# Optimization experiments

Measured on AMD Instinct MI355X. Metric: run time of the kernel, lower is better.

The kernel has to match this reference:

```python
import jax, jax.numpy as jnp
import numpy as np

DIM = 2048
H = 256
N_HEADS = 4
HEAD_DIM = H // N_HEADS
N_SIG = 6
SW_HID = 2 * DIM  # SwiGLU(dim, dim*2)
B, S = 4, 2048
EPS = 1e-6


def _rmsnorm(v, w):
    return v * jax.lax.rsqrt(jnp.mean(v * v, axis=-1, keepdims=True) + EPS) * w


def setup_inputs() -> dict:
    key = jax.random.key(0)
    ks = jax.random.split(key, 32)
    sc = 0.02
    inp = {
        'x': jax.random.normal(ks[0], (B, S, DIM), jnp.float32),
        'epistemic': jax.random.uniform(ks[1], (B, 64), jnp.float32),
        'aleatoric': jax.random.uniform(ks[2], (B, 64), jnp.float32),
        'ood_score': jax.random.uniform(ks[3], (B,), jnp.float32),
        'conformal_unc': jax.random.uniform(ks[4], (B,), jnp.float32),
        'ece': jax.random.uniform(ks[5], (1,), jnp.float32),
        'moral_std': jax.random.uniform(ks[6], (B,), jnp.float32),
        # signal_proj: Linear(1, h)
        'sp_w': jax.random.normal(ks[7], (H, 1), jnp.float32) * sc,
        'sp_b': jnp.zeros((H,), jnp.float32),
        # MultiheadAttention packed qkv + out proj
        'in_proj_w': jax.random.normal(ks[8], (3 * H, H), jnp.float32) * sc,
        'in_proj_b': jnp.zeros((3 * H,), jnp.float32),
        'out_w': jax.random.normal(ks[9], (H, H), jnp.float32) * sc,
        'out_b': jnp.zeros((H,), jnp.float32),
        # confidence_head: Linear(6,h) -> GELU -> Linear(h,1) -> Sigmoid
        'ch_w1': jax.random.normal(ks[10], (H, N_SIG), jnp.float32) * sc,
        'ch_b1': jnp.zeros((H,), jnp.float32),
        'ch_w2': jax.random.normal(ks[11], (1, H), jnp.float32) * sc,
        'ch_b2': jnp.zeros((1,), jnp.float32),
        # summary_proj: Linear(h,dim) -> RMSNorm -> SwiGLU(dim, 2*dim) -> Linear(dim,dim) -> RMSNorm
        'sum_w1': jax.random.normal(ks[12], (DIM, H), jnp.float32) * sc,
        'sum_b1': jnp.zeros((DIM,), jnp.float32),
        'rms1_w': jnp.ones((DIM,), jnp.float32),
        'sw_w1': jax.random.normal(ks[13], (SW_HID, DIM), jnp.float32) * sc,
        'sw_w3': jax.random.normal(ks[14], (SW_HID, DIM), jnp.float32) * sc,
        'sw_w2': jax.random.normal(ks[15], (DIM, SW_HID), jnp.float32) * sc,
        'sum_w2': jax.random.normal(ks[16], (DIM, DIM), jnp.float32) * sc,
        'sum_b2': jnp.zeros((DIM,), jnp.float32),
        'rms2_w': jnp.ones((DIM,), jnp.float32),
        # final norm
        'norm_w': jnp.ones((DIM,), jnp.float32),
    }
    return inp


def reference(x, epistemic, aleatoric, ood_score, conformal_unc, ece, moral_std,
              sp_w, sp_b, in_proj_w, in_proj_b, out_w, out_b,
              ch_w1, ch_b1, ch_w2, ch_b2,
              sum_w1, sum_b1, rms1_w, sw_w1, sw_w3, sw_w2, sum_w2, sum_b2, rms2_w,
              norm_w):
    b, s, d = x.shape
    # [B, 6] stack of scalar uncertainty signals
    signals = jnp.stack([
        epistemic.mean(-1), aleatoric.mean(-1), ood_score, conformal_unc,
        jnp.broadcast_to(ece, (b,)), moral_std], axis=-1)
    # confidence head: Linear -> GELU(exact) -> Linear -> Sigmoid
    c = jax.nn.gelu(signals @ ch_w1.T + ch_b1, approximate=False)
    confidence = jax.nn.sigmoid(c @ ch_w2.T + ch_b2)[..., 0]
    # project each scalar signal to h dims: [B, 6, H]
    sp = signals[..., None] * sp_w[:, 0] + sp_b
    # self-attention over the 6 signal tokens
    qkv = sp @ in_proj_w.T + in_proj_b            # [B, 6, 3H]
    q, k, v = jnp.split(qkv, 3, axis=-1)
    q = q.reshape(b, N_SIG, N_HEADS, HEAD_DIM)
    k = k.reshape(b, N_SIG, N_HEADS, HEAD_DIM)
    v = v.reshape(b, N_SIG, N_HEADS, HEAD_DIM)
    scores = jnp.einsum('bqhd,bkhd->bhqk', q, k) / jnp.sqrt(jnp.float32(HEAD_DIM))
    attn = jax.nn.softmax(scores, axis=-1)
    o = jnp.einsum('bhqk,bkhd->bqhd', attn, v).reshape(b, N_SIG, H)
    o = o @ out_w.T + out_b
    unc_summary = o.mean(axis=1)                   # [B, H]
    # summary_proj applied (as in the original) to the [B*S, H] expanded rows
    u = jnp.broadcast_to(unc_summary[:, None, :], (b, s, H)).reshape(b * s, H)
    t = u @ sum_w1.T + sum_b1                      # [B*S, DIM]
    t = _rmsnorm(t, rms1_w)
    t = (jax.nn.silu(t @ sw_w1.T) * (t @ sw_w3.T)) @ sw_w2.T  # SwiGLU
    t = t @ sum_w2.T + sum_b2
    unc_embedding = _rmsnorm(t, rms2_w).reshape(b, s, d)
    x_aware = _rmsnorm(x + unc_embedding * 0.05, norm_w)
    return (x_aware, confidence, signals, unc_embedding)
```

## Files before the change

kernel.cpp:

```cpp
#include <hip/hip_runtime.h>
#include <math.h>

#define DIMN 2048
#define HDIM 256
#define NSIG 6
#define NHEADS 4
#define HEADDIM 64
#define SWHID 4096
#define BB 4
#define SSEQ 2048
#define EPSF 1e-6f

__device__ __forceinline__ float wsum(float v) {
    #pragma unroll
    for (int m = 1; m < 64; m <<= 1) v += __shfl_xor(v, m, 64);
    return v;
}

__device__ __forceinline__ float dot4(float4 a, float4 b) {
    return a.x*b.x + a.y*b.y + a.z*b.z + a.w*b.w;
}

__global__ __launch_bounds__(256) void k0_ac(
    const float* __restrict__ ipw, const float* __restrict__ ipb,
    const float* __restrict__ spw, const float* __restrict__ spb,
    float* __restrict__ A, float* __restrict__ C, float* __restrict__ accum)
{
    int t = threadIdx.x, wv = t >> 6, lane = t & 63;
    if (blockIdx.x == 0 && t < 8) accum[t] = 0.f;
    int r = blockIdx.x * 4 + wv;
    float4 w  = ((const float4*)(ipw + (size_t)r * HDIM))[lane];
    float4 a4 = ((const float4*)spw)[lane];
    float4 b4 = ((const float4*)spb)[lane];
    float aa = wsum(dot4(w, a4));
    float cc = wsum(dot4(w, b4));
    if (lane == 0) { A[r] = aa; C[r] = cc + ipb[r]; }
}

__global__ __launch_bounds__(256) void kUV(
    const float* __restrict__ A, const float* __restrict__ C,
    const float* __restrict__ outw,
    float* __restrict__ U, float* __restrict__ V)
{
    int t = threadIdx.x, wv = t >> 6, lane = t & 63;
    int n = blockIdx.x * 4 + wv;
    float4 w = ((const float4*)(outw + (size_t)n * HDIM))[lane];
    float4 a = ((const float4*)(A + 512))[lane];
    float4 c = ((const float4*)(C + 512))[lane];
    float pu = dot4(w, a), pv = dot4(w, c);
    #pragma unroll
    for (int m = 1; m < 16; m <<= 1) {
        pu += __shfl_xor(pu, m, 64);
        pv += __shfl_xor(pv, m, 64);
    }
    if ((lane & 15) == 0) {
        int h = lane >> 4;
        U[n * NHEADS + h] = pu;
        V[n * NHEADS + h] = pv;
    }
}

__global__ __launch_bounds__(256) void kB_front(
    const float* __restrict__ epi, const float* __restrict__ ale,
    const float* __restrict__ ood, const float* __restrict__ cunc,
    const float* __restrict__ ece, const float* __restrict__ moral,
    const float* __restrict__ chw1, const float* __restrict__ chb1,
    const float* __restrict__ chw2, const float* __restrict__ chb2,
    const float* __restrict__ A, const float* __restrict__ C,
    const float* __restrict__ U, const float* __restrict__ V,
    const float* __restrict__ outb,
    float* __restrict__ us, float* __restrict__ out_conf,
    float* __restrict__ out_sig)
{
    __shared__ float sA[512], sC[512];
    __shared__ float sSig[BB][NSIG];
    __shared__ float sGram[NHEADS][4];
    __shared__ float sAtt[BB][NHEADS][NSIG][NSIG];
    __shared__ float sBar[BB][NHEADS][NSIG];
    __shared__ float sRedW[BB][4];
    int t = threadIdx.x, wv = t >> 6, lane = t & 63;

    for (int r = t; r < 512; r += 256) { sA[r] = A[r]; sC[r] = C[r]; }

    {
        int b = wv;
        float se = wsum(epi[b * 64 + lane]) * (1.f / 64.f);
        float sa = wsum(ale[b * 64 + lane]) * (1.f / 64.f);
        if (lane == 0) {
            sSig[b][0] = se; sSig[b][1] = sa;
            sSig[b][2] = ood[b]; sSig[b][3] = cunc[b];
            sSig[b][4] = ece[0]; sSig[b][5] = moral[b];
            #pragma unroll
            for (int k = 0; k < NSIG; k++) out_sig[b * NSIG + k] = sSig[b][k];
        }
    }
    __syncthreads();

    {
        int h = wv;
        float aq = sA[h * 64 + lane],       cq = sC[h * 64 + lane];
        float ak = sA[256 + h * 64 + lane], ck = sC[256 + h * 64 + lane];
        float g0 = wsum(aq * ak);
        float g1 = wsum(aq * ck);
        float g2 = wsum(cq * ak);
        float g3 = wsum(cq * ck);
        if (lane == 0) { sGram[h][0] = g0; sGram[h][1] = g1; sGram[h][2] = g2; sGram[h][3] = g3; }
    }

    {
        float c1[NSIG];
        #pragma unroll
        for (int j = 0; j < NSIG; j++) c1[j] = chw1[t * NSIG + j];
        float cb = chb1[t], cw2 = chw2[t];
        #pragma unroll
        for (int b = 0; b < BB; b++) {
            float z = cb;
            #pragma unroll
            for (int j = 0; j < NSIG; j++) z += sSig[b][j] * c1[j];
            float g = 0.5f * z * (1.f + erff(z * 0.70710678118654752f));
            float v = wsum(g * cw2);
            if (lane == 0) sRedW[b][wv] = v;
        }
    }
    __syncthreads();
    if (t < BB) {
        float s = sRedW[t][0] + sRedW[t][1] + sRedW[t][2] + sRedW[t][3] + chb2[0];
        out_conf[t] = 1.f / (1.f + expf(-s));
    }

    if (t < 96) {
        int b = t / 24, r = t % 24, h = r / 6, qi = r % 6;
        float sq = sSig[b][qi];
        float g0 = sGram[h][0], g1 = sGram[h][1], g2 = sGram[h][2], g3 = sGram[h][3];
        float sc[NSIG]; float mx = -1e30f;
        #pragma unroll
        for (int ki = 0; ki < NSIG; ki++) {
            float sk = sSig[b][ki];
            float s = (g0 * sq * sk + g1 * sq + g2 * sk + g3) * 0.125f;
            sc[ki] = s; mx = fmaxf(mx, s);
        }
        float den = 0;
        #pragma unroll
        for (int ki = 0; ki < NSIG; ki++) { sc[ki] = expf(sc[ki] - mx); den += sc[ki]; }
        float inv = 1.f / den;
        #pragma unroll
        for (int ki = 0; ki < NSIG; ki++) sAtt[b][h][qi][ki] = sc[ki] * inv;
    }
    __syncthreads();

    if (t < 96) {
        int b = t / 24, r = t % 24, h = r / 6, ki = r % 6;
        float s = 0;
        #pragma unroll
        for (int qi = 0; qi < NSIG; qi++) s += sAtt[b][h][qi][ki];
        sBar[b][h][ki] = s * (1.f / 6.f);
    }
    __syncthreads();

    {
        float uu[NHEADS], vv[NHEADS];
        #pragma unroll
        for (int h = 0; h < NHEADS; h++) {
            uu[h] = U[t * NHEADS + h];
            vv[h] = V[t * NHEADS + h];
        }
        float ob = outb[t];
        #pragma unroll
        for (int b = 0; b < BB; b++) {
            float acc = ob;
            #pragma unroll
            for (int h = 0; h < NHEADS; h++) {
                float hu = 0, hv = 0;
                #pragma unroll
                for (int ki = 0; ki < NSIG; ki++) {
                    hu += sBar[b][h][ki] * sSig[b][ki];
                    hv += sBar[b][h][ki];
                }
                acc += hu * uu[h] + hv * vv[h];
            }
            us[b * HDIM + t] = acc;
        }
    }
}

__global__ __launch_bounds__(256) void k2_sumproj(
    const float* __restrict__ us, const float* __restrict__ w1,
    const float* __restrict__ b1, const float* __restrict__ rw1,
    float* __restrict__ t1n, float* __restrict__ accum)
{
    __shared__ float bsq[BB];
    int t = threadIdx.x, wv = t >> 6, lane = t & 63;
    if (t < BB) bsq[t] = 0.f;
    __syncthreads();
    int d = blockIdx.x * 4 + wv;
    float4 w = ((const float4*)(w1 + (size_t)d * HDIM))[lane];
    float acc[BB];
    #pragma unroll
    for (int b = 0; b < BB; b++) {
        float4 u = ((const float4*)(us + b * HDIM))[lane];
        acc[b] = dot4(w, u);
    }
    #pragma unroll
    for (int b = 0; b < BB; b++) acc[b] = wsum(acc[b]);
    if (lane == 0) {
        #pragma unroll
        for (int b = 0; b < BB; b++) {
            float v = acc[b] + b1[d];
            atomicAdd(&bsq[b], v * v);
            t1n[b * DIMN + d] = v * rw1[d];
        }
    }
    __syncthreads();
    if (t < BB) atomicAdd(&accum[t], bsq[t]);
}

__global__ __launch_bounds__(256) void k3_swiglu(
    const float* __restrict__ t1n, const float* __restrict__ sw1,
    const float* __restrict__ sw3, const float* __restrict__ accum,
    float* __restrict__ h)
{
    __shared__ __align__(16) float sT[BB * DIMN];
    int t = threadIdx.x, wv = t >> 6, lane = t & 63;
    #pragma unroll
    for (int k = 0; k < 8; k++)
        ((float4*)sT)[k * 256 + t] = ((const float4*)t1n)[k * 256 + t];
    __syncthreads();
    int j = blockIdx.x * 4 + wv;
    const float4* r1 = (const float4*)(sw1 + (size_t)j * DIMN);
    const float4* r3 = (const float4*)(sw3 + (size_t)j * DIMN);
    float acc1[BB] = {0,0,0,0}, acc3[BB] = {0,0,0,0};
    #pragma unroll
    for (int it = 0; it < 8; it++) {
        float4 w1 = r1[it * 64 + lane];
        float4 w3 = r3[it * 64 + lane];
        #pragma unroll
        for (int b = 0; b < BB; b++) {
            float4 tv = ((const float4*)(sT + b * DIMN))[it * 64 + lane];
            acc1[b] += dot4(w1, tv);
            acc3[b] += dot4(w3, tv);
        }
    }
    #pragma unroll
    for (int b = 0; b < BB; b++) { acc1[b] = wsum(acc1[b]); acc3[b] = wsum(acc3[b]); }
    if (lane == 0) {
        #pragma unroll
        for (int b = 0; b < BB; b++) {
            float s = rsqrtf(accum[b] * (1.f / DIMN) + EPSF);
            float a = acc1[b] * s;
            float sil = a / (1.f + expf(-a));
            h[b * SWHID + j] = sil * (acc3[b] * s);
        }
    }
}

__global__ __launch_bounds__(256) void k4_down(
    const float* __restrict__ h, const float* __restrict__ sw2,
    float* __restrict__ t2)
{
    __shared__ __align__(16) float sH[BB * SWHID];
    int t = threadIdx.x, wv = t >> 6, lane = t & 63;
    #pragma unroll
    for (int k = 0; k < 16; k++)
        ((float4*)sH)[k * 256 + t] = ((const float4*)h)[k * 256 + t];
    __syncthreads();
    int d = blockIdx.x * 4 + wv;
    const float4* wr = (const float4*)(sw2 + (size_t)d * SWHID);
    float acc[BB] = {0,0,0,0};
    #pragma unroll
    for (int it = 0; it < 16; it++) {
        float4 w = wr[it * 64 + lane];
        #pragma unroll
        for (int b = 0; b < BB; b++) {
            float4 hv = ((const float4*)(sH + b * SWHID))[it * 64 + lane];
            acc[b] += dot4(w, hv);
        }
    }
    #pragma unroll
    for (int b = 0; b < BB; b++) acc[b] = wsum(acc[b]);
    if (lane == 0) {
        #pragma unroll
        for (int b = 0; b < BB; b++) t2[b * DIMN + d] = acc[b];
    }
}

__global__ __launch_bounds__(256) void k5_out(
    const float* __restrict__ t2, const float* __restrict__ w2,
    const float* __restrict__ b2, const float* __restrict__ rw2,
    float* __restrict__ t3n, float* __restrict__ accum)
{
    __shared__ __align__(16) float sT[BB * DIMN];
    __shared__ float bsq[BB];
    int t = threadIdx.x, wv = t >> 6, lane = t & 63;
    if (t < BB) bsq[t] = 0.f;
    #pragma unroll
    for (int k = 0; k < 8; k++)
        ((float4*)sT)[k * 256 + t] = ((const float4*)t2)[k * 256 + t];
    __syncthreads();
    int d = blockIdx.x * 4 + wv;
    const float4* wr = (const float4*)(w2 + (size_t)d * DIMN);
    float acc[BB] = {0,0,0,0};
    #pragma unroll
    for (int it = 0; it < 8; it++) {
        float4 w = wr[it * 64 + lane];
        #pragma unroll
        for (int b = 0; b < BB; b++) {
            float4 tv = ((const float4*)(sT + b * DIMN))[it * 64 + lane];
            acc[b] += dot4(w, tv);
        }
    }
    #pragma unroll
    for (int b = 0; b < BB; b++) acc[b] = wsum(acc[b]);
    if (lane == 0) {
        #pragma unroll
        for (int b = 0; b < BB; b++) {
            float v = acc[b] + b2[d];
            atomicAdd(&bsq[b], v * v);
            t3n[b * DIMN + d] = v * rw2[d];
        }
    }
    __syncthreads();
    if (t < BB) atomicAdd(&accum[4 + t], bsq[t]);
}

__global__ __launch_bounds__(256) void k7_final(
    const float* __restrict__ x, const float* __restrict__ t3n,
    const float* __restrict__ accum, const float* __restrict__ nw,
    float* __restrict__ xa, float* __restrict__ ue)
{
    int t = threadIdx.x, wv = t >> 6, lane = t & 63;
    size_t row = (size_t)blockIdx.x * 4 + wv;
    int b = (int)(row >> 11);
    float scale2 = rsqrtf(accum[4 + b] * (1.f / DIMN) + EPSF);
    const float4* xr = (const float4*)(x + row * DIMN);
    const float4* tr = (const float4*)(t3n + (size_t)b * DIMN);
    float4 e[8], y[8];
    float ss = 0.f;
    #pragma unroll
    for (int k = 0; k < 8; k++) {
        int idx = k * 64 + lane;
        float4 tv = tr[idx];
        float4 xv = xr[idx];
        e[k].x = tv.x * scale2; e[k].y = tv.y * scale2;
        e[k].z = tv.z * scale2; e[k].w = tv.w * scale2;
        y[k].x = xv.x + 0.05f * e[k].x; y[k].y = xv.y + 0.05f * e[k].y;
        y[k].z = xv.z + 0.05f * e[k].z; y[k].w = xv.w + 0.05f * e[k].w;
        ss += dot4(y[k], y[k]);
    }
    float rs = rsqrtf(wsum(ss) * (1.f / DIMN) + EPSF);
    float4* xo = (float4*)(xa + row * DIMN);
    float4* uo = (float4*)(ue + row * DIMN);
    #pragma unroll
    for (int k = 0; k < 8; k++) {
        int idx = k * 64 + lane;
        float4 nv = ((const float4*)nw)[idx];
        float4 o;
        o.x = y[k].x * rs * nv.x; o.y = y[k].y * rs * nv.y;
        o.z = y[k].z * rs * nv.z; o.w = y[k].w * rs * nv.w;
        xo[idx] = o;
        uo[idx] = e[k];
    }
}

extern "C" void kernel_launch(void* const* d_in, const int* in_sizes, int n_in,
                              void* d_out, int out_size, void* d_ws, size_t ws_size,
                              hipStream_t stream)
{
    (void)in_sizes; (void)n_in; (void)out_size; (void)ws_size;
    const float* x     = (const float*)d_in[0];
    const float* epi   = (const float*)d_in[1];
    const float* ale   = (const float*)d_in[2];
    const float* ood   = (const float*)d_in[3];
    const float* cunc  = (const float*)d_in[4];
    const float* ece   = (const float*)d_in[5];
    const float* moral = (const float*)d_in[6];
    const float* spw   = (const float*)d_in[7];
    const float* spb   = (const float*)d_in[8];
    const float* ipw   = (const float*)d_in[9];
    const float* ipb   = (const float*)d_in[10];
    const float* outw  = (const float*)d_in[11];
    const float* outb  = (const float*)d_in[12];
    const float* chw1  = (const float*)d_in[13];
    const float* chb1  = (const float*)d_in[14];
    const float* chw2  = (const float*)d_in[15];
    const float* chb2  = (const float*)d_in[16];
    const float* sumw1 = (const float*)d_in[17];
    const float* sumb1 = (const float*)d_in[18];
    const float* rms1  = (const float*)d_in[19];
    const float* sww1  = (const float*)d_in[20];
    const float* sww3  = (const float*)d_in[21];
    const float* sww2  = (const float*)d_in[22];
    const float* sumw2 = (const float*)d_in[23];
    const float* sumb2 = (const float*)d_in[24];
    const float* rms2  = (const float*)d_in[25];
    const float* normw = (const float*)d_in[26];

    float* out  = (float*)d_out;
    float* xa   = out;
    float* conf = out + (size_t)BB * SSEQ * DIMN;
    float* sig  = conf + BB;
    float* ue   = sig + BB * NSIG;

    float* ws    = (float*)d_ws;
    float* A     = ws;
    float* C     = ws + 768;
    float* U     = ws + 1536;
    float* V     = ws + 2560;
    float* us    = ws + 3584;
    float* t1n   = ws + 4608;
    float* h     = ws + 12800;
    float* t2    = ws + 29184;
    float* t3n   = ws + 37376;
    float* accum = ws + 45568;

    k0_ac   <<<192, 256, 0, stream>>>(ipw, ipb, spw, spb, A, C, accum);
    kUV     <<<64, 256, 0, stream>>>(A, C, outw, U, V);
    kB_front<<<1, 256, 0, stream>>>(epi, ale, ood, cunc, ece, moral,
                                    chw1, chb1, chw2, chb2, A, C, U, V, outb,
                                    us, conf, sig);
    k2_sumproj<<<512, 256, 0, stream>>>(us, sumw1, sumb1, rms1, t1n, accum);
    k3_swiglu <<<1024, 256, 0, stream>>>(t1n, sww1, sww3, accum, h);
    k4_down   <<<512, 256, 0, stream>>>(h, sww2, t2);
    k5_out    <<<512, 256, 0, stream>>>(t2, sumw2, sumb2, rms2, t3n, accum);
    k7_final  <<<2048, 256, 0, stream>>>(x, t3n, accum, normw, xa, ue);
}
```

Before: 354.1 us.

## Fuse weight-chain kernels into one persistent kernel with grid barriers and prefetch

Merges the front attention, sum projection, SwiGLU, down projection and output projection kernels into a single 512-block persistent kernel. Stages are separated by atomic grid-wide barriers, and idle warps in the early small stages prefetch the SwiGLU weights into cache. The out-projection is reorganised to go through a head-weighted vector g followed by one matvec. This removes several kernel launch gaps and overlaps weight loading with the serial front work. In exchange it depends on all 512 blocks being co-resident (launch bounds of 2 blocks per CU), which risks deadlock, and adds the cost of the spin barriers.

```diff
diff --git a/kernel.cpp b/kernel.cpp
--- a/kernel.cpp
+++ b/kernel.cpp
@@ -10,6 +10,7 @@
 #define BB 4
 #define SSEQ 2048
 #define EPSF 1e-6f
+#define NBLK 512
 
 __device__ __forceinline__ float wsum(float v) {
     #pragma unroll
@@ -21,305 +22,319 @@
     return a.x*b.x + a.y*b.y + a.z*b.z + a.w*b.w;
 }
 
-__global__ __launch_bounds__(256) void k0_ac(
-    const float* __restrict__ ipw, const float* __restrict__ ipb,
-    const float* __restrict__ spw, const float* __restrict__ spb,
-    float* __restrict__ A, float* __restrict__ C, float* __restrict__ accum)
+__device__ __forceinline__ void gsync(unsigned* bar) {
+    __syncthreads();
+    if (threadIdx.x == 0) {
+        __hip_atomic_fetch_add(bar, 1u, __ATOMIC_RELEASE,
+                               __HIP_MEMORY_SCOPE_AGENT);
+        while (__hip_atomic_load(bar, __ATOMIC_ACQUIRE,
+                                 __HIP_MEMORY_SCOPE_AGENT) < NBLK) {
+            __builtin_amdgcn_s_sleep(2);
+        }
+    }
+    __syncthreads();
+}
+
+struct Params {
+    const float *ipw, *ipb, *spw, *spb;
+    const float *epi, *ale, *ood, *cunc, *ece, *moral;
+    const float *chw1, *chb1, *chw2, *chb2;
+    const float *outw, *outb;
+    const float *sumw1, *sumb1, *rms1;
+    const float *sww1, *sww3, *sww2;
+    const float *sumw2, *sumb2, *rms2;
+    float *A, *C, *g, *us, *t1n, *h, *t2, *t3n, *accum;
+    float *conf, *sig;
+    unsigned *bar;
+};
+
+__global__ __launch_bounds__(256) void kinit(float* accum, unsigned* bar) {
+    int t = threadIdx.x;
+    if (t < 8) accum[t] = 0.f;
+    bar[t] = 0u;
+}
+
+__device__ __forceinline__ void pf8k(const float* sww1, const float* sww3,
+                                     int c, int lane) {
+    if (c >= 8192) return;
+    const float* base = (c < 4096) ? (sww1 + (size_t)c * 2048)
+                                   : (sww3 + (size_t)(c - 4096) * 2048);
+    const float4* p4 = (const float4*)base;
+    float s = 0.f;
+    #pragma unroll
+    for (int k = 0; k < 8; k++) {
+        float4 v = p4[k * 64 + lane];
+        s += v.x + v.y + v.z + v.w;
+    }
+    asm volatile("" :: "v"(s));
+}
+
+__global__ __launch_bounds__(256, 2) void kchain(Params p)
 {
+    __shared__ __align__(16) float smem[16384];
     int t = threadIdx.x, wv = t >> 6, lane = t & 63;
-    if (blockIdx.x == 0 && t < 8) accum[t] = 0.f;
-    int r = blockIdx.x * 4 + wv;
-    float4 w  = ((const float4*)(ipw + (size_t)r * HDIM))[lane];
-    float4 a4 = ((const float4*)spw)[lane];
-    float4 b4 = ((const float4*)spb)[lane];
-    float aa = wsum(dot4(w, a4));
-    float cc = wsum(dot4(w, b4));
-    if (lane == 0) { A[r] = aa; C[r] = cc + ipb[r]; }
-}
-
-__global__ __launch_bounds__(256) void kUV(
-    const float* __restrict__ A, const float* __restrict__ C,
-    const float* __restrict__ outw,
-    float* __restrict__ U, float* __restrict__ V)
-{
-    int t = threadIdx.x, wv = t >> 6, lane = t & 63;
-    int n = blockIdx.x * 4 + wv;
-    float4 w = ((const float4*)(outw + (size_t)n * HDIM))[lane];
-    float4 a = ((const float4*)(A + 512))[lane];
-    float4 c = ((const float4*)(C + 512))[lane];
-    float pu = dot4(w, a), pv = dot4(w, c);
-    #pragma unroll
-    for (int m = 1; m < 16; m <<= 1) {
-        pu += __shfl_xor(pu, m, 64);
-        pv += __shfl_xor(pv, m, 64);
-    }
-    if ((lane & 15) == 0) {
-        int h = lane >> 4;
-        U[n * NHEADS + h] = pu;
-        V[n * NHEADS + h] = pv;
-    }
-}
-
-__global__ __launch_bounds__(256) void kB_front(
-    const float* __restrict__ epi, const float* __restrict__ ale,
-    const float* __restrict__ ood, const float* __restrict__ cunc,
-    const float* __restrict__ ece, const float* __restrict__ moral,
-    const float* __restrict__ chw1, const float* __restrict__ chb1,
-    const float* __restrict__ chw2, const float* __restrict__ chb2,
-    const float* __restrict__ A, const float* __restrict__ C,
-    const float* __restrict__ U, const float* __restrict__ V,
-    const float* __restrict__ outb,
-    float* __restrict__ us, float* __restrict__ out_conf,
-    float* __restrict__ out_sig)
-{
-    __shared__ float sA[512], sC[512];
-    __shared__ float sSig[BB][NSIG];
-    __shared__ float sGram[NHEADS][4];
-    __shared__ float sAtt[BB][NHEADS][NSIG][NSIG];
-    __shared__ float sBar[BB][NHEADS][NSIG];
-    __shared__ float sRedW[BB][4];
-    int t = threadIdx.x, wv = t >> 6, lane = t & 63;
-
-    for (int r = t; r < 512; r += 256) { sA[r] = A[r]; sC[r] = C[r]; }
+    int gw = blockIdx.x * 4 + wv;
+
+    if (gw < 768) {
+        int r = gw;
+        float4 w  = ((const float4*)(p.ipw + (size_t)r * HDIM))[lane];
+        float4 a4 = ((const float4*)p.spw)[lane];
+        float4 b4 = ((const float4*)p.spb)[lane];
+        float aa = wsum(dot4(w, a4));
+        float cc = wsum(dot4(w, b4));
+        if (lane == 0) { p.A[r] = aa; p.C[r] = cc + p.ipb[r]; }
+    } else {
+        pf8k(p.sww1, p.sww3, gw - 768, lane);
+    }
+    gsync(p.bar + 0 * 32);
+
+    if (blockIdx.x == 0) {
+        float* sA   = smem;
+        float* sC   = smem + 768;
+        float* sSig = smem + 1536;
+        float* sGram= smem + 1568;
+        float* sAtt = smem + 1600;
+        float* sBar = smem + 2176;
+        float* sRedW= smem + 2272;
+        float* sHu  = smem + 2288;
+        float* sHv  = smem + 2304;
+
+        for (int r = t; r < 768; r += 256) { sA[r] = p.A[r]; sC[r] = p.C[r]; }
+
+        {
+            int b = wv;
+            float se = wsum(p.epi[b * 64 + lane]) * (1.f / 64.f);
+            float sa = wsum(p.ale[b * 64 + lane]) * (1.f / 64.f);
+            if (lane == 0) {
+                sSig[b*6+0] = se; sSig[b*6+1] = sa;
+                sSig[b*6+2] = p.ood[b]; sSig[b*6+3] = p.cunc[b];
+                sSig[b*6+4] = p.ece[0]; sSig[b*6+5] = p.moral[b];
+                #pragma unroll
+                for (int k = 0; k < NSIG; k++) p.sig[b*6+k] = sSig[b*6+k];
+            }
+        }
+        __syncthreads();
+
+        {
+            int h = wv;
+            float aq = sA[h*64+lane],       cq = sC[h*64+lane];
+            float ak = sA[256+h*64+lane],   ck = sC[256+h*64+lane];
+            float g0 = wsum(aq*ak), g1 = wsum(aq*ck);
+            float g2 = wsum(cq*ak), g3 = wsum(cq*ck);
+            if (lane == 0) { sGram[h*4+0]=g0; sGram[h*4+1]=g1;
+                             sGram[h*4+2]=g2; sGram[h*4+3]=g3; }
+        }
+
+        {
+            float c1[NSIG];
+            #pragma unroll
+            for (int j = 0; j < NSIG; j++) c1[j] = p.chw1[t*NSIG+j];
+            float cb = p.chb1[t], cw2 = p.chw2[t];
+            #pragma unroll
+            for (int b = 0; b < BB; b++) {
+                float z = cb;
+                #pragma unroll
+                for (int j = 0; j < NSIG; j++) z += sSig[b*6+j] * c1[j];
+                float gg = 0.5f * z * (1.f + erff(z * 0.70710678118654752f));
+                float v = wsum(gg * cw2);
+                if (lane == 0) sRedW[b*4+wv] = v;
+            }
+        }
+        __syncthreads();
+        if (t < BB) {
+            float s = sRedW[t*4+0]+sRedW[t*4+1]+sRedW[t*4+2]+sRedW[t*4+3]
+                    + p.chb2[0];
+            p.conf[t] = 1.f / (1.f + expf(-s));
+        }
+
+        if (t < 96) {
+            int b = t / 24, r = t % 24, h = r / 6, qi = r % 6;
+            float sq = sSig[b*6+qi];
+            float g0=sGram[h*4+0], g1=sGram[h*4+1];
+            float g2=sGram[h*4+2], g3=sGram[h*4+3];
+            float sc[NSIG]; float mx = -1e30f;
+            #pragma unroll
+            for (int ki = 0; ki < NSIG; ki++) {
+                float sk = sSig[b*6+ki];
+                float s = (g0*sq*sk + g1*sq + g2*sk + g3) * 0.125f;
+                sc[ki] = s; mx = fmaxf(mx, s);
+            }
+            float den = 0;
+            #pragma unroll
+            for (int ki = 0; ki < NSIG; ki++) { sc[ki] = expf(sc[ki]-mx); den += sc[ki]; }
+            float inv = 1.f / den;
+            #pragma unroll
+            for (int ki = 0; ki < NSIG; ki++)
+                sAtt[((b*4+h)*6+qi)*6+ki] = sc[ki] * inv;
+        }
+        __syncthreads();
+
+        if (t < 96) {
+            int b = t / 24, r = t % 24, h = r / 6, ki = r % 6;
+            float s = 0;
+            #pragma unroll
+            for (int qi = 0; qi < NSIG; qi++) s += sAtt[((b*4+h)*6+qi)*6+ki];
+            sBar[(b*4+h)*6+ki] = s * (1.f / 6.f);
+        }
+        __syncthreads();
+
+        if (t < 16) {
+            int b = t >> 2, h = t & 3;
+            float hu = 0, hv = 0;
+            #pragma unroll
+            for (int ki = 0; ki < NSIG; ki++) {
+                float a = sBar[(b*4+h)*6+ki];
+                hu += a * sSig[b*6+ki]; hv += a;
+            }
+            sHu[b*4+h] = hu; sHv[b*4+h] = hv;
+        }
+        __syncthreads();
+
+        {
+            int m = t, hh = m >> 6;
+            #pragma unroll
+            for (int b = 0; b < BB; b++)
+                p.g[b*HDIM+m] = sHu[b*4+hh]*sA[512+m] + sHv[b*4+hh]*sC[512+m];
+        }
+    } else {
+        pf8k(p.sww1, p.sww3, 1280 + (gw - 4), lane);
+    }
+    gsync(p.bar + 1 * 32);
+
+    if (gw < HDIM) {
+        int n = gw;
+        float4 w = ((const float4*)(p.outw + (size_t)n * HDIM))[lane];
+        float ob = p.outb[n];
+        #pragma unroll
+        for (int b = 0; b < BB; b++) {
+            float4 g4 = ((const float4*)(p.g + b * HDIM))[lane];
+            float acc = wsum(dot4(w, g4));
+            if (lane == 0) p.us[b * HDIM + n] = acc + ob;
+        }
+    } else {
+        pf8k(p.sww1, p.sww3, 3324 + (gw - 256), lane);
+    }
+    gsync(p.bar + 2 * 32);
 
     {
-        int b = wv;
-        float se = wsum(epi[b * 64 + lane]) * (1.f / 64.f);
-        float sa = wsum(ale[b * 64 + lane]) * (1.f / 64.f);
+        float* sred = smem + 12288;
+        if (t < BB) sred[t] = 0.f;
+        __syncthreads();
+        int d = gw;
+        float4 w = ((const float4*)(p.sumw1 + (size_t)d * HDIM))[lane];
+        float acc[BB];
+        #pragma unroll
+        for (int b = 0; b < BB; b++)
+            acc[b] = dot4(w, ((const float4*)(p.us + b * HDIM))[lane]);
+        #pragma unroll
+        for (int b = 0; b < BB; b++) acc[b] = wsum(acc[b]);
         if (lane == 0) {
-            sSig[b][0] = se; sSig[b][1] = sa;
-            sSig[b][2] = ood[b]; sSig[b][3] = cunc[b];
-            sSig[b][4] = ece[0]; sSig[b][5] = moral[b];
-            #pragma unroll
-            for (int k = 0; k < NSIG; k++) out_sig[b * NSIG + k] = sSig[b][k];
-        }
-    }
-    __syncthreads();
+            #pragma unroll
+            for (int b = 0; b < BB; b++) {
+                float v = acc[b] + p.sumb1[d];
+                atomicAdd(&sred[b], v * v);
+                p.t1n[b * DIMN + d] = v * p.rms1[d];
+            }
+        }
+        __syncthreads();
+        if (t < BB) atomicAdd(&p.accum[t], sred[t]);
+    }
+    gsync(p.bar + 3 * 32);
 
     {
-        int h = wv;
-        float aq = sA[h * 64 + lane],       cq = sC[h * 64 + lane];
-        float ak = sA[256 + h * 64 + lane], ck = sC[256 + h * 64 + lane];
-        float g0 = wsum(aq * ak);
-        float g1 = wsum(aq * ck);
-        float g2 = wsum(cq * ak);
-        float g3 = wsum(cq * ck);
-        if (lane == 0) { sGram[h][0] = g0; sGram[h][1] = g1; sGram[h][2] = g2; sGram[h][3] = g3; }
-    }
+        #pragma unroll
+        for (int k = 0; k < 8; k++)
+            ((float4*)smem)[k * 256 + t] = ((const float4*)p.t1n)[k * 256 + t];
+        __syncthreads();
+        float s1[BB];
+        #pragma unroll
+        for (int b = 0; b < BB; b++)
+            s1[b] = rsqrtf(p.accum[b] * (1.f / DIMN) + EPSF);
+        #pragma unroll
+        for (int jj = 0; jj < 2; jj++) {
+            int j = blockIdx.x * 8 + wv * 2 + jj;
+            const float4* r1 = (const float4*)(p.sww1 + (size_t)j * DIMN);
+            const float4* r3 = (const float4*)(p.sww3 + (size_t)j * DIMN);
+            float a1[BB] = {0,0,0,0}, a3[BB] = {0,0,0,0};
+            #pragma unroll
+            for (int it = 0; it < 8; it++) {
+                float4 w1 = r1[it * 64 + lane];
+                float4 w3 = r3[it * 64 + lane];
+                #pragma unroll
+                for (int b = 0; b < BB; b++) {
+                    float4 tv = ((const float4*)(smem + b * DIMN))[it * 64 + lane];
+                    a1[b] += dot4(w1, tv);
+                    a3[b] += dot4(w3, tv);
+                }
+            }
+            #pragma unroll
+            for (int b = 0; b < BB; b++) { a1[b] = wsum(a1[b]); a3[b] = wsum(a3[b]); }
+            if (lane == 0) {
+                #pragma unroll
+                for (int b = 0; b < BB; b++) {
+                    float a = a1[b] * s1[b];
+                    float sil = a / (1.f + expf(-a));
+                    p.h[b * SWHID + j] = sil * (a3[b] * s1[b]);
+                }
+            }
+        }
+    }
+    gsync(p.bar + 4 * 32);
 
     {
-        float c1[NSIG];
-        #pragma unroll
-        for (int j = 0; j < NSIG; j++) c1[j] = chw1[t * NSIG + j];
-        float cb = chb1[t], cw2 = chw2[t];
-        #pragma unroll
-        for (int b = 0; b < BB; b++) {
-            float z = cb;
-            #pragma unroll
-            for (int j = 0; j < NSIG; j++) z += sSig[b][j] * c1[j];
-            float g = 0.5f * z * (1.f + erff(z * 0.70710678118654752f));
-            float v = wsum(g * cw2);
-            if (lane == 0) sRedW[b][wv] = v;
-        }
-    }
-    __syncthreads();
-    if (t < BB) {
-        float s = sRedW[t][0] + sRedW[t][1] + sRedW[t][2] + sRedW[t][3] + chb2[0];
-        out_conf[t] = 1.f / (1.f + expf(-s));
-    }
-
-    if (t < 96) {
-        int b = t / 24, r = t % 24, h = r / 6, qi = r % 6;
-        float sq = sSig[b][qi];
-        float g0 = sGram[h][0], g1 = sGram[h][1], g2 = sGram[h][2], g3 = sGram[h][3];
-        float sc[NSIG]; float mx = -1e30f;
-        #pragma unroll
-        for (int ki = 0; ki < NSIG; ki++) {
-            float sk = sSig[b][ki];
-            float s = (g0 * sq * sk + g1 * sq + g2 * sk + g3) * 0.125f;
-            sc[ki] = s; mx = fmaxf(mx, s);
-        }
-        float den = 0;
-        #pragma unroll
-        for (int ki = 0; ki < NSIG; ki++) { sc[ki] = expf(sc[ki] - mx); den += sc[ki]; }
-        float inv = 1.f / den;
-        #pragma unroll
-        for (int ki = 0; ki < NSIG; ki++) sAtt[b][h][qi][ki] = sc[ki] * inv;
-    }
-    __syncthreads();
-
-    if (t < 96) {
-        int b = t / 24, r = t % 24, h = r / 6, ki = r % 6;
-        float s = 0;
-        #pragma unroll
-        for (int qi = 0; qi < NSIG; qi++) s += sAtt[b][h][qi][ki];
-        sBar[b][h][ki] = s * (1.f / 6.f);
-    }
-    __syncthreads();
+        #pragma unroll
+        for (int k = 0; k < 16; k++)
+            ((float4*)smem)[k * 256 + t] = ((const float4*)p.h)[k * 256 + t];
+        __syncthreads();
+        int d = gw;
+        const float4* wr = (const float4*)(p.sww2 + (size_t)d * SWHID);
+        float acc[BB] = {0,0,0,0};
+        #pragma unroll
+        for (int it = 0; it < 16; it++) {
+            float4 w = wr[it * 64 + lane];
+            #pragma unroll
+            for (int b = 0; b < BB; b++)
+                acc[b] += dot4(w, ((const float4*)(smem + b * SWHID))[it * 64 + lane]);
+        }
+        #pragma unroll
+        for (int b = 0; b < BB; b++) acc[b] = wsum(acc[b]);
+        if (lane == 0) {
+            #pragma unroll
+            for (int b = 0; b < BB; b++) p.t2[b * DIMN + d] = acc[b];
+        }
+    }
+    gsync(p.bar + 5 * 32);
 
     {
-        float uu[NHEADS], vv[NHEADS];
-        #pragma unroll
-        for (int h = 0; h < NHEADS; h++) {
-            uu[h] = U[t * NHEADS + h];
-            vv[h] = V[t * NHEADS + h];
-        }
-        float ob = outb[t];
-        #pragma unroll
-        for (int b = 0; b < BB; b++) {
-            float acc = ob;
-            #pragma unroll
-            for (int h = 0; h < NHEADS; h++) {
-                float hu = 0, hv = 0;
-                #pragma unroll
-                for (int ki = 0; ki < NSIG; ki++) {
-                    hu += sBar[b][h][ki] * sSig[b][ki];
-                    hv += sBar[b][h][ki];
-                }
-                acc += hu * uu[h] + hv * vv[h];
-            }
-            us[b * HDIM + t] = acc;
-        }
-    }
-}
-
-__global__ __launch_bounds__(256) void k2_sumproj(
-    const float* __restrict__ us, const float* __restrict__ w1,
-    const float* __restrict__ b1, const float* __restrict__ rw1,
-    float* __restrict__ t1n, float* __restrict__ accum)
-{
-    __shared__ float bsq[BB];
-    int t = threadIdx.x, wv = t >> 6, lane = t & 63;
-    if (t < BB) bsq[t] = 0.f;
-    __syncthreads();
-    int d = blockIdx.x * 4 + wv;
-    float4 w = ((const float4*)(w1 + (size_t)d * HDIM))[lane];
-    float acc[BB];
-    #pragma unroll
-    for (int b = 0; b < BB; b++) {
-        float4 u = ((const float4*)(us + b * HDIM))[lane];
-        acc[b] = dot4(w, u);
-    }
-    #pragma unroll
-    for (int b = 0; b < BB; b++) acc[b] = wsum(acc[b]);
-    if (lane == 0) {
-        #pragma unroll
-        for (int b = 0; b < BB; b++) {
-            float v = acc[b] + b1[d];
-            atomicAdd(&bsq[b], v * v);
-            t1n[b * DIMN + d] = v * rw1[d];
-        }
-    }
-    __syncthreads();
-    if (t < BB) atomicAdd(&accum[t], bsq[t]);
-}
-
-__global__ __launch_bounds__(256) void k3_swiglu(
-    const float* __restrict__ t1n, const float* __restrict__ sw1,
-    const float* __restrict__ sw3, const float* __restrict__ accum,
-    float* __restrict__ h)
-{
-    __shared__ __align__(16) float sT[BB * DIMN];
-    int t = threadIdx.x, wv = t >> 6, lane = t & 63;
-    #pragma unroll
-    for (int k = 0; k < 8; k++)
-        ((float4*)sT)[k * 256 + t] = ((const float4*)t1n)[k * 256 + t];
-    __syncthreads();
-    int j = blockIdx.x * 4 + wv;
-    const float4* r1 = (const float4*)(sw1 + (size_t)j * DIMN);
-    const float4* r3 = (const float4*)(sw3 + (size_t)j * DIMN);
-    float acc1[BB] = {0,0,0,0}, acc3[BB] = {0,0,0,0};
-    #pragma unroll
-    for (int it = 0; it < 8; it++) {
-        float4 w1 = r1[it * 64 + lane];
-        float4 w3 = r3[it * 64 + lane];
-        #pragma unroll
-        for (int b = 0; b < BB; b++) {
-            float4 tv = ((const float4*)(sT + b * DIMN))[it * 64 + lane];
-            acc1[b] += dot4(w1, tv);
-            acc3[b] += dot4(w3, tv);
-        }
-    }
-    #pragma unroll
-    for (int b = 0; b < BB; b++) { acc1[b] = wsum(acc1[b]); acc3[b] = wsum(acc3[b]); }
-    if (lane == 0) {
-        #pragma unroll
-        for (int b = 0; b < BB; b++) {
-            float s = rsqrtf(accum[b] * (1.f / DIMN) + EPSF);
-            float a = acc1[b] * s;
-            float sil = a / (1.f + expf(-a));
-            h[b * SWHID + j] = sil * (acc3[b] * s);
-        }
-    }
-}
-
-__global__ __launch_bounds__(256) void k4_down(
-    const float* __restrict__ h, const float* __restrict__ sw2,
-    float* __restrict__ t2)
-{
-    __shared__ __align__(16) float sH[BB * SWHID];
-    int t = threadIdx.x, wv = t >> 6, lane = t & 63;
-    #pragma unroll
-    for (int k = 0; k < 16; k++)
-        ((float4*)sH)[k * 256 + t] = ((const float4*)h)[k * 256 + t];
-    __syncthreads();
-    int d = blockIdx.x * 4 + wv;
-    const float4* wr = (const float4*)(sw2 + (size_t)d * SWHID);
-    float acc[BB] = {0,0,0,0};
-    #pragma unroll
-    for (int it = 0; it < 16; it++) {
-        float4 w = wr[it * 64 + lane];
-        #pragma unroll
-        for (int b = 0; b < BB; b++) {
-            float4 hv = ((const float4*)(sH + b * SWHID))[it * 64 + lane];
-            acc[b] += dot4(w, hv);
-        }
-    }
-    #pragma unroll
-    for (int b = 0; b < BB; b++) acc[b] = wsum(acc[b]);
-    if (lane == 0) {
-        #pragma unroll
-        for (int b = 0; b < BB; b++) t2[b * DIMN + d] = acc[b];
-    }
-}
-
-__global__ __launch_bounds__(256) void k5_out(
-    const float* __restrict__ t2, const float* __restrict__ w2,
-    const float* __restrict__ b2, const float* __restrict__ rw2,
-    float* __restrict__ t3n, float* __restrict__ accum)
-{
-    __shared__ __align__(16) float sT[BB * DIMN];
-    __shared__ float bsq[BB];
-    int t = threadIdx.x, wv = t >> 6, lane = t & 63;
-    if (t < BB) bsq[t] = 0.f;
-    #pragma unroll
-    for (int k = 0; k < 8; k++)
-        ((float4*)sT)[k * 256 + t] = ((const float4*)t2)[k * 256 + t];
-    __syncthreads();
-    int d = blockIdx.x * 4 + wv;
-    const float4* wr = (const float4*)(w2 + (size_t)d * DIMN);
-    float acc[BB] = {0,0,0,0};
-    #pragma unroll
-    for (int it = 0; it < 8; it++) {
-        float4 w = wr[it * 64 + lane];
-        #pragma unroll
-        for (int b = 0; b < BB; b++) {
-            float4 tv = ((const float4*)(sT + b * DIMN))[it * 64 + lane];
-            acc[b] += dot4(w, tv);
-        }
-    }
-    #pragma unroll
-    for (int b = 0; b < BB; b++) acc[b] = wsum(acc[b]);
-    if (lane == 0) {
-        #pragma unroll
-        for (int b = 0; b < BB; b++) {
-            float v = acc[b] + b2[d];
-            atomicAdd(&bsq[b], v * v);
-            t3n[b * DIMN + d] = v * rw2[d];
-        }
-    }
-    __syncthreads();
-    if (t < BB) atomicAdd(&accum[4 + t], bsq[t]);
+        float* sred = smem + 12288;
+        if (t < BB) sred[t] = 0.f;
+        #pragma unroll
+        for (int k = 0; k < 8; k++)
+            ((float4*)smem)[k * 256 + t] = ((const float4*)p.t2)[k * 256 + t];
+        __syncthreads();
+        int d = gw;
+        const float4* wr = (const float4*)(p.sumw2 + (size_t)d * DIMN);
+        float acc[BB] = {0,0,0,0};
+        #pragma unroll
+        for (int it = 0; it < 8; it++) {
+            float4 w = wr[it * 64 + lane];
+            #pragma unroll
+            for (int b = 0; b < BB; b++)
+                acc[b] += dot4(w, ((const float4*)(smem + b * DIMN))[it * 64 + lane]);
+        }
+        #pragma unroll
+        for (int b = 0; b < BB; b++) acc[b] = wsum(acc[b]);
+        if (lane == 0) {
+            #pragma unroll
+            for (int b = 0; b < BB; b++) {
+                float v = acc[b] + p.sumb2[d];
+                atomicAdd(&sred[b], v * v);
+                p.t3n[b * DIMN + d] = v * p.rms2[d];
+            }
+        }
+        __syncthreads();
+        if (t < BB) atomicAdd(&p.accum[4 + t], sred[t]);
+    }
 }
 
 __global__ __launch_bounds__(256) void k7_final(
@@ -367,32 +382,6 @@
 {
     (void)in_sizes; (void)n_in; (void)out_size; (void)ws_size;
     const float* x     = (const float*)d_in[0];
-    const float* epi   = (const float*)d_in[1];
-    const float* ale   = (const float*)d_in[2];
-    const float* ood   = (const float*)d_in[3];
-    const float* cunc  = (const float*)d_in[4];
-    const float* ece   = (const float*)d_in[5];
-    const float* moral = (const float*)d_in[6];
-    const float* spw   = (const float*)d_in[7];
-    const float* spb   = (const float*)d_in[8];
-    const float* ipw   = (const float*)d_in[9];
-    const float* ipb   = (const float*)d_in[10];
-    const float* outw  = (const float*)d_in[11];
-    const float* outb  = (const float*)d_in[12];
-    const float* chw1  = (const float*)d_in[13];
-    const float* chb1  = (const float*)d_in[14];
-    const float* chw2  = (const float*)d_in[15];
-    const float* chb2  = (const float*)d_in[16];
-    const float* sumw1 = (const float*)d_in[17];
-    const float* sumb1 = (const float*)d_in[18];
-    const float* rms1  = (const float*)d_in[19];
-    const float* sww1  = (const float*)d_in[20];
-    const float* sww3  = (const float*)d_in[21];
-    const float* sww2  = (const float*)d_in[22];
-    const float* sumw2 = (const float*)d_in[23];
-    const float* sumb2 = (const float*)d_in[24];
-    const float* rms2  = (const float*)d_in[25];
-    const float* normw = (const float*)d_in[26];
 
     float* out  = (float*)d_out;
     float* xa   = out;
@@ -400,26 +389,50 @@
     float* sig  = conf + BB;
     float* ue   = sig + BB * NSIG;
 
-    float* ws    = (float*)d_ws;
-    float* A     = ws;
-    float* C     = ws + 768;
-    float* U     = ws + 1536;
-    float* V     = ws + 2560;
-    float* us    = ws + 3584;
-    float* t1n   = ws + 4608;
-    float* h     = ws + 12800;
-    float* t2    = ws + 29184;
-    float* t3n   = ws + 37376;
-    float* accum = ws + 45568;
-
-    k0_ac   <<<192, 256, 0, stream>>>(ipw, ipb, spw, spb, A, C, accum);
-    kUV     <<<64, 256, 0, stream>>>(A, C, outw, U, V);
-    kB_front<<<1, 256, 0, stream>>>(epi, ale, ood, cunc, ece, moral,
-                                    chw1, chb1, chw2, chb2, A, C, U, V, outb,
-                                    us, conf, sig);
-    k2_sumproj<<<512, 256, 0, stream>>>(us, sumw1, sumb1, rms1, t1n, accum);
-    k3_swiglu <<<1024, 256, 0, stream>>>(t1n, sww1, sww3, accum, h);
-    k4_down   <<<512, 256, 0, stream>>>(h, sww2, t2);
-    k5_out    <<<512, 256, 0, stream>>>(t2, sumw2, sumb2, rms2, t3n, accum);
-    k7_final  <<<2048, 256, 0, stream>>>(x, t3n, accum, normw, xa, ue);
-}
+    float* ws = (float*)d_ws;
+
+    Params hp;
+    hp.ipw   = (const float*)d_in[9];
+    hp.ipb   = (const float*)d_in[10];
+    hp.spw   = (const float*)d_in[7];
+    hp.spb   = (const float*)d_in[8];
+    hp.epi   = (const float*)d_in[1];
+    hp.ale   = (const float*)d_in[2];
+    hp.ood   = (const float*)d_in[3];
+    hp.cunc  = (const float*)d_in[4];
+    hp.ece   = (const float*)d_in[5];
+    hp.moral = (const float*)d_in[6];
+    hp.chw1  = (const float*)d_in[13];
+    hp.chb1  = (const float*)d_in[14];
+    hp.chw2  = (const float*)d_in[15];
+    hp.chb2  = (const float*)d_in[16];
+    hp.outw  = (const float*)d_in[11];
+    hp.outb  = (const float*)d_in[12];
+    hp.sumw1 = (const float*)d_in[17];
+    hp.sumb1 = (const float*)d_in[18];
+    hp.rms1  = (const float*)d_in[19];
+    hp.sww1  = (const float*)d_in[20];
+    hp.sww3  = (const float*)d_in[21];
+    hp.sww2  = (const float*)d_in[22];
+    hp.sumw2 = (const float*)d_in[23];
+    hp.sumb2 = (const float*)d_in[24];
+    hp.rms2  = (const float*)d_in[25];
+
+    hp.A     = ws;
+    hp.C     = ws + 768;
+    hp.g     = ws + 1536;
+    hp.us    = ws + 2560;
+    hp.t1n   = ws + 3584;
+    hp.h     = ws + 11776;
+    hp.t2    = ws + 28160;
+    hp.t3n   = ws + 36352;
+    hp.accum = ws + 44544;
+    hp.bar   = (unsigned*)(ws + 44800);
+    hp.conf  = conf;
+    hp.sig   = sig;
+
+    kinit<<<1, 256, 0, stream>>>(hp.accum, hp.bar);
+    kchain<<<NBLK, 256, 0, stream>>>(hp);
+    k7_final<<<2048, 256, 0, stream>>>(x, hp.t3n, hp.accum,
+                                       (const float*)d_in[26], xa, ue);
+}
```

Result: slower. 606.6 us (+71.3%).
